# Kernel tuning notes

Measured on AMD Instinct MI355X. Metric: run time of the kernel, lower is better.

Reference implementation:

```python
import jax, jax.numpy as jnp
import numpy as np

B, S, D, P = 8, 2048, 512, 64  # batch, seq, num_embed_hidden, num_attention_project


def setup_inputs() -> dict:
    key = jax.random.key(0)
    ks = jax.random.split(key, 9)
    sd = 1.0 / np.sqrt(D)
    sp = 1.0 / np.sqrt(P)
    return {
        "query": jax.random.normal(ks[0], (B, S, D), dtype=jnp.float32),
        "attention_mask": jnp.ones((B, S), dtype=jnp.float32),
        "Wq": jax.random.uniform(ks[1], (D, P), jnp.float32, -sd, sd),
        "bq": jax.random.uniform(ks[2], (P,), jnp.float32, -sd, sd),
        "Wk": jax.random.uniform(ks[3], (D, P), jnp.float32, -sd, sd),
        "bk": jax.random.uniform(ks[4], (P,), jnp.float32, -sd, sd),
        "Wv": jax.random.uniform(ks[5], (D, P), jnp.float32, -sd, sd),
        "bv": jax.random.uniform(ks[6], (P,), jnp.float32, -sd, sd),
        "Wo": jax.random.uniform(ks[7], (P, D), jnp.float32, -sp, sp),
        "bo": jax.random.uniform(ks[8], (D,), jnp.float32, -sp, sp),
    }


def reference(query, attention_mask, Wq, bq, Wk, bk, Wv, bv, Wo, bo):
    q = jnp.einsum("bsd,dp->bsp", query, Wq) + bq  # [B,S,P]
    k = jnp.einsum("bsd,dp->bsp", query, Wk) + bk
    v = jnp.einsum("bsd,dp->bsp", query, Wv) + bv
    scores = jnp.einsum("bsp,btp->bst", q, k) / jnp.sqrt(jnp.float32(P))  # [B,S,S]
    # Faithful to original: mask broadcast over last axis via unsqueeze(-1) -> masks rows
    scores = scores + (1.0 - attention_mask[:, :, None]) * -10000.0
    weights = jax.nn.softmax(scores, axis=-1)
    weighted = jnp.einsum("bst,btp->bsp", weights, v)
    return jnp.einsum("bsp,pd->bsd", weighted, Wo) + bo
```

## Files before the change

kernel.cpp:

```cpp
#include <hip/hip_runtime.h>
#include <hip/hip_bf16.h>
#include <math.h>

constexpr int B = 8;
constexpr int S = 2048;
constexpr int D = 512;
constexpr int P = 64;
constexpr float SCALE = 0.125f;

typedef short bf16x8 __attribute__((ext_vector_type(8)));
typedef float f32x4 __attribute__((ext_vector_type(4)));
typedef unsigned int u32;

__device__ __forceinline__ unsigned short f2bf(float x) {
  __hip_bfloat16 h = __float2bfloat16(x);
  return __builtin_bit_cast(unsigned short, h);
}
__device__ __forceinline__ float bf2f(unsigned short u) {
  unsigned int v = (unsigned int)u << 16;
  return __builtin_bit_cast(float, v);
}


__global__ __launch_bounds__(256) void prep_w(
    const float* __restrict__ Wq, const float* __restrict__ Wk,
    const float* __restrict__ Wv, const float* __restrict__ Wo,
    unsigned short* __restrict__ Bfrag, unsigned short* __restrict__ Wofrag) {
  const int i = blockIdx.x * 256 + threadIdx.x;
  if (i < 192 * 512) {
    const int d = i / 192;
    const int n = i - d * 192;
    const float* W = (n < 64) ? Wq : (n < 128) ? Wk : Wv;
    const float val = W[d * 64 + (n & 63)];
    const int nt = n >> 4, l15 = n & 15;
    const int k16 = d >> 5, l4 = (d >> 3) & 3, j = d & 7;
    Bfrag[(((nt * 16 + k16) * 4 + l4) * 16 + l15) * 8 + j] = f2bf(val);
  }
  if (i < 64 * 512) {
    const int k = i >> 9;
    const int n = i & 511;
    const float val = Wo[k * 512 + n];
    const int ct = n >> 4, l15 = n & 15;
    const int h = k >> 5, l4 = (k >> 3) & 3, j = k & 7;
    Wofrag[(((ct * 2 + h) * 4 + l4) * 16 + l15) * 8 + j] = f2bf(val);
  }
}

__global__ __launch_bounds__(256, 4) void qkv_mfma(
    const float* __restrict__ query, const unsigned short* __restrict__ Bfrag,
    const float* __restrict__ bq, const float* __restrict__ bk,
    const float* __restrict__ bv, unsigned short* __restrict__ qfrag,
    unsigned short* __restrict__ kfrag, unsigned short* __restrict__ vfrag) {
  __shared__ __align__(16) unsigned short Aq[16 * 512];

  const int tid = threadIdx.x;
  const int w = tid >> 6;
  const int l = tid & 63;
  const int l15 = l & 15;
  const int l4 = l >> 4;
  const int s0 = blockIdx.x * 16;

  const float* qsrc = query + (size_t)s0 * D;
#pragma unroll
  for (int step = 0; step < 4; ++step) {
    const int row = step * 4 + w;
    const float* pf = qsrc + row * D + l * 8;
    const float4 x = *(const float4*)pf;
    const float4 y = *(const float4*)(pf + 4);
    bf16x8 u;
    u[0] = (short)f2bf(x.x); u[1] = (short)f2bf(x.y);
    u[2] = (short)f2bf(x.z); u[3] = (short)f2bf(x.w);
    u[4] = (short)f2bf(y.x); u[5] = (short)f2bf(y.y);
    u[6] = (short)f2bf(y.z); u[7] = (short)f2bf(y.w);
    *(bf16x8*)&Aq[row * 512 + ((l ^ (row & 7)) << 3)] = u;
  }
  __syncthreads();

  f32x4 acc[3];
#pragma unroll
  for (int nt = 0; nt < 3; ++nt) acc[nt] = (f32x4){0.f, 0.f, 0.f, 0.f};

#pragma unroll
  for (int k16 = 0; k16 < 16; ++k16) {
    const int aslot = (k16 * 4 + l4) ^ (l15 & 7);
    const bf16x8 af = *(const bf16x8*)&Aq[l15 * 512 + (aslot << 3)];
#pragma unroll
    for (int nt = 0; nt < 3; ++nt) {
      const int ntg = w * 3 + nt;
      const bf16x8 bf =
          *(const bf16x8*)(Bfrag + ((size_t)(ntg * 16 + k16) * 64 + l) * 8);
      acc[nt] = __builtin_amdgcn_mfma_f32_16x16x32_bf16(af, bf, acc[nt], 0, 0,
                                                        0);
    }
  }

  const int b = s0 >> 11;
  const size_t bbase = (size_t)b * (S * P);
#pragma unroll
  for (int nt = 0; nt < 3; ++nt) {
    const int col = w * 48 + nt * 16 + l15;
    const int mat = col >> 6;
    const int p = col & 63;
    const float bb = ((mat == 0) ? bq : (mat == 1) ? bk : bv)[p];
#pragma unroll
    for (int r = 0; r < 4; ++r) {
      const int s = s0 + l4 * 4 + r;
      const int t = s & 2047;
      const float vl = acc[nt][r] + bb;
      if (mat == 2) {
        const int tb = t >> 5, chv = (t >> 3) & 3, jv = t & 7;
        const int pcv = p >> 4, rowv = p & 15;
        vfrag[bbase + (((size_t)(tb * 4 + pcv) * 4 + chv) * 16 + rowv) * 8 +
              jv] = f2bf(vl);
      } else {
        const int tile = t >> 4, rowin = t & 15;
        const int h = p >> 5, chp = (p >> 3) & 3, j = p & 7;
        unsigned short* dst = (mat == 0) ? qfrag : kfrag;
        dst[bbase + (((size_t)(tile * 2 + h) * 4 + chp) * 16 + rowin) * 8 +
            j] = f2bf(mat == 0 ? vl * SCALE : vl);
      }
    }
  }
}

__global__ __launch_bounds__(512, 4) void attn_fused(
    const unsigned short* __restrict__ qfrag,
    const unsigned short* __restrict__ kfrag,
    const unsigned short* __restrict__ vfrag,
    const unsigned short* __restrict__ Wofrag, const float* __restrict__ bo,
    float* __restrict__ out) {
  __shared__ __align__(16) unsigned char smem[57344];
  __shared__ float l_s[8][32];

  const int tid = threadIdx.x;
  const int w = tid >> 6;
  const int lane = tid & 63;
  const int l15 = lane & 15;
  const int l4 = lane >> 4;
  const int qg = w & 1;
  const int th = w >> 1;

  const int blk = blockIdx.x;
  const int b = blk & 7;
  const int s0 = (blk >> 3) * 64;

  const size_t bbase = (size_t)b * (S * P);
  const unsigned short* qf = qfrag + bbase;
  const unsigned short* kf = kfrag + bbase;
  const unsigned short* vf = vfrag + bbase;

  unsigned short* e_s = (unsigned short*)smem + w * 2048;

  bf16x8 aq[2][2];
#pragma unroll
  for (int st = 0; st < 2; ++st)
#pragma unroll
    for (int h = 0; h < 2; ++h)
      aq[st][h] = *(const bf16x8*)(qf +
                                   ((size_t)(((s0 >> 4) + qg * 2 + st) * 2 + h) *
                                        64 +
                                    lane) *
                                       8);

  f32x4 acc[2][4];
#pragma unroll
  for (int st = 0; st < 2; ++st)
#pragma unroll
    for (int pc = 0; pc < 4; ++pc) acc[st][pc] = (f32x4){0.f, 0.f, 0.f, 0.f};
  float lpart[2][4] = {{0.f, 0.f, 0.f, 0.f}, {0.f, 0.f, 0.f, 0.f}};

  for (int win = 0; win < 8; ++win) {
    const int t0 = th * 512 + win * 64;

    bf16x8 bk[4][2];
#pragma unroll
    for (int nt = 0; nt < 4; ++nt)
#pragma unroll
      for (int h = 0; h < 2; ++h)
        bk[nt][h] =
            *(const bf16x8*)(kf +
                             ((size_t)(((t0 >> 4) + nt) * 2 + h) * 64 + lane) *
                                 8);

    f32x4 sc[2][4];
#pragma unroll
    for (int st = 0; st < 2; ++st)
#pragma unroll
      for (int nt = 0; nt < 4; ++nt) {
        f32x4 c = (f32x4){0.f, 0.f, 0.f, 0.f};
        c = __builtin_amdgcn_mfma_f32_16x16x32_bf16(aq[st][0], bk[nt][0], c, 0,
                                                    0, 0);
        sc[st][nt] = __builtin_amdgcn_mfma_f32_16x16x32_bf16(
            aq[st][1], bk[nt][1], c, 0, 0, 0);
      }

    bf16x8 bv[4][2];
#pragma unroll
    for (int pc = 0; pc < 4; ++pc)
#pragma unroll
      for (int kk = 0; kk < 2; ++kk)
        bv[pc][kk] =
            *(const bf16x8*)(vf +
                             ((size_t)(((t0 >> 5) + kk) * 4 + pc) * 64 + lane) *
                                 8);

#pragma unroll
    for (int st = 0; st < 2; ++st)
#pragma unroll
      for (int nt = 0; nt < 4; ++nt) {
        const int ch = nt * 2 + (l15 >> 3);
#pragma unroll
        for (int r = 0; r < 4; ++r) {
          const int rr = l4 * 4 + r;
          const unsigned short eu = f2bf(__expf(sc[st][nt][r]));
          lpart[st][r] += bf2f(eu);
          e_s[st * 1024 + rr * 64 + ((ch ^ (rr & 7)) << 3) + (l15 & 7)] = eu;
        }
      }

#pragma unroll
    for (int st = 0; st < 2; ++st) {
      bf16x8 ae[2];
#pragma unroll
      for (int kk = 0; kk < 2; ++kk)
        ae[kk] = *(const bf16x8*)&e_s[st * 1024 + l15 * 64 +
                                      (((kk * 4 + l4) ^ (l15 & 7)) << 3)];
#pragma unroll
      for (int pc = 0; pc < 4; ++pc) {
        acc[st][pc] = __builtin_amdgcn_mfma_f32_16x16x32_bf16(
            ae[0], bv[pc][0], acc[st][pc], 0, 0, 0);
        acc[st][pc] = __builtin_amdgcn_mfma_f32_16x16x32_bf16(
            ae[1], bv[pc][1], acc[st][pc], 0, 0, 0);
      }
    }
  }

#pragma unroll
  for (int st = 0; st < 2; ++st)
#pragma unroll
    for (int r = 0; r < 4; ++r) {
      float v = lpart[st][r];
      v += __shfl_xor(v, 1, 64);
      v += __shfl_xor(v, 2, 64);
      v += __shfl_xor(v, 4, 64);
      v += __shfl_xor(v, 8, 64);
      if (l15 == 0) l_s[w][st * 16 + l4 * 4 + r] = v;
    }

  __syncthreads();

  float* pacc = (float*)smem;
  if (th > 0) {
#pragma unroll
    for (int st = 0; st < 2; ++st)
#pragma unroll
      for (int pc = 0; pc < 4; ++pc)
#pragma unroll
        for (int r = 0; r < 4; ++r)
          pacc[((size_t)(qg * 3 + th - 1) * 32 + st * 16 + l4 * 4 + r) * 64 +
               pc * 16 + l15] = acc[st][pc][r];
  }
  __syncthreads();

  unsigned short* wnorm = (unsigned short*)(smem + 49152);
  if (th == 0) {
#pragma unroll
    for (int st = 0; st < 2; ++st) {
      float rl[4];
#pragma unroll
      for (int r = 0; r < 4; ++r) {
        const int row = st * 16 + l4 * 4 + r;
        rl[r] = 1.f / (l_s[qg][row] + l_s[2 + qg][row] + l_s[4 + qg][row] +
                       l_s[6 + qg][row]);
      }
#pragma unroll
      for (int pc = 0; pc < 4; ++pc)
#pragma unroll
        for (int r = 0; r < 4; ++r) {
          float s = acc[st][pc][r];
#pragma unroll
          for (int j = 0; j < 3; ++j)
            s += pacc[((size_t)(qg * 3 + j) * 32 + st * 16 + l4 * 4 + r) * 64 +
                      pc * 16 + l15];
          wnorm[(qg * 32 + st * 16 + l4 * 4 + r) * 64 + pc * 16 + l15] =
              f2bf(s * rl[r]);
        }
    }
  }
  __syncthreads();

  const int sub = w & 3;
  const int chalf = w >> 2;
  const bf16x8 a0 = *(const bf16x8*)&wnorm[(sub * 16 + l15) * 64 + l4 * 8];
  const bf16x8 a1 =
      *(const bf16x8*)&wnorm[(sub * 16 + l15) * 64 + 32 + l4 * 8];
  const size_t orow0 = (size_t)b * S + s0 + sub * 16;
#pragma unroll
  for (int ct = 0; ct < 16; ++ct) {
    const int ctg = chalf * 16 + ct;
    const bf16x8 b0 =
        *(const bf16x8*)(Wofrag + ((size_t)(ctg * 2 + 0) * 64 + lane) * 8);
    const bf16x8 b1 =
        *(const bf16x8*)(Wofrag + ((size_t)(ctg * 2 + 1) * 64 + lane) * 8);
    f32x4 c = (f32x4){0.f, 0.f, 0.f, 0.f};
    c = __builtin_amdgcn_mfma_f32_16x16x32_bf16(a0, b0, c, 0, 0, 0);
    c = __builtin_amdgcn_mfma_f32_16x16x32_bf16(a1, b1, c, 0, 0, 0);
    const int col = ctg * 16 + l15;
    const float bb = bo[col];
#pragma unroll
    for (int r = 0; r < 4; ++r)
      out[(orow0 + l4 * 4 + r) * D + col] = c[r] + bb;
  }
}

extern "C" void kernel_launch(void* const* d_in, const int* in_sizes, int n_in,
                              void* d_out, int out_size, void* d_ws,
                              size_t ws_size, hipStream_t stream) {
  const float* query = (const float*)d_in[0];
  const float* Wq = (const float*)d_in[2];
  const float* bq = (const float*)d_in[3];
  const float* Wk = (const float*)d_in[4];
  const float* bk = (const float*)d_in[5];
  const float* Wv = (const float*)d_in[6];
  const float* bv = (const float*)d_in[7];
  const float* Wo = (const float*)d_in[8];
  const float* bo = (const float*)d_in[9];
  float* out = (float*)d_out;

  const size_t proj = (size_t)B * S * P;
  unsigned short* qfr = (unsigned short*)d_ws;
  unsigned short* kfr = qfr + proj;
  unsigned short* vfr = kfr + proj;
  unsigned short* Bfrag = vfr + proj;
  unsigned short* Wofrag = Bfrag + 192 * 512;

  prep_w<<<384, 256, 0, stream>>>(Wq, Wk, Wv, Wo, Bfrag, Wofrag);
  qkv_mfma<<<1024, 256, 0, stream>>>(query, Bfrag, bq, bk, bv, qfr, kfr, vfr);
  attn_fused<<<256, 512, 0, stream>>>(qfr, kfr, vfr, Wofrag, bo, out);
}
```

Baseline: 142.4 us.

## Double attention block to 16 waves splitting keys eight ways, stagger access order

The attention kernel now runs 1024 threads per block, so 16 waves split each 64-query tile's keys eight ways instead of four. Each wave handles four 64-key windows and writes its exp tile into a double-buffered LDS region, with the score and exp steps interleaved per query subtile. Window order, QKV k-order and output column order are rotated per block to spread concurrent global/L2 accesses. LDS grows to about 128 KB per block, which limits residency to one block per CU and adds a larger cross-wave partial-sum reduction.

```diff
diff --git a/kernel.cpp b/kernel.cpp
--- a/kernel.cpp
+++ b/kernel.cpp
@@ -59,6 +59,7 @@
   const int l15 = l & 15;
   const int l4 = l >> 4;
   const int s0 = blockIdx.x * 16;
+  const int kb0 = blockIdx.x & 15;
 
   const float* qsrc = query + (size_t)s0 * D;
 #pragma unroll
@@ -81,7 +82,8 @@
   for (int nt = 0; nt < 3; ++nt) acc[nt] = (f32x4){0.f, 0.f, 0.f, 0.f};
 
 #pragma unroll
-  for (int k16 = 0; k16 < 16; ++k16) {
+  for (int kk = 0; kk < 16; ++kk) {
+    const int k16 = (kk + kb0) & 15;
     const int aslot = (k16 * 4 + l4) ^ (l15 & 7);
     const bf16x8 af = *(const bf16x8*)&Aq[l15 * 512 + (aslot << 3)];
 #pragma unroll
@@ -123,14 +125,14 @@
   }
 }
 
-__global__ __launch_bounds__(512, 4) void attn_fused(
+__global__ __launch_bounds__(1024, 4) void attn_fused(
     const unsigned short* __restrict__ qfrag,
     const unsigned short* __restrict__ kfrag,
     const unsigned short* __restrict__ vfrag,
     const unsigned short* __restrict__ Wofrag, const float* __restrict__ bo,
     float* __restrict__ out) {
-  __shared__ __align__(16) unsigned char smem[57344];
-  __shared__ float l_s[8][32];
+  __shared__ __align__(16) unsigned char smem[131072];
+  __shared__ float l_s[16][32];
 
   const int tid = threadIdx.x;
   const int w = tid >> 6;
@@ -142,25 +144,27 @@
 
   const int blk = blockIdx.x;
   const int b = blk & 7;
-  const int s0 = (blk >> 3) * 64;
+  const int qt = blk >> 3;
+  const int s0 = qt * 64;
+  const int wst = qt & 3;
 
   const size_t bbase = (size_t)b * (S * P);
   const unsigned short* qf = qfrag + bbase;
   const unsigned short* kf = kfrag + bbase;
   const unsigned short* vf = vfrag + bbase;
 
-  unsigned short* e_s = (unsigned short*)smem + w * 2048;
+  unsigned short* e_w = (unsigned short*)smem + w * 4096;
 
   bf16x8 aq[2][2];
 #pragma unroll
   for (int st = 0; st < 2; ++st)
 #pragma unroll
     for (int h = 0; h < 2; ++h)
-      aq[st][h] = *(const bf16x8*)(qf +
-                                   ((size_t)(((s0 >> 4) + qg * 2 + st) * 2 + h) *
-                                        64 +
-                                    lane) *
-                                       8);
+      aq[st][h] =
+          *(const bf16x8*)(qf +
+                           ((size_t)(((s0 >> 4) + qg * 2 + st) * 2 + h) * 64 +
+                            lane) *
+                               8);
 
   f32x4 acc[2][4];
 #pragma unroll
@@ -169,8 +173,10 @@
     for (int pc = 0; pc < 4; ++pc) acc[st][pc] = (f32x4){0.f, 0.f, 0.f, 0.f};
   float lpart[2][4] = {{0.f, 0.f, 0.f, 0.f}, {0.f, 0.f, 0.f, 0.f}};
 
-  for (int win = 0; win < 8; ++win) {
-    const int t0 = th * 512 + win * 64;
+  for (int win = 0; win < 4; ++win) {
+    const int wi = (win + wst) & 3;
+    const int t0 = th * 256 + wi * 64;
+    unsigned short* e_s = e_w + (win & 1) * 2048;
 
     bf16x8 bk[4][2];
 #pragma unroll
@@ -182,17 +188,29 @@
                              ((size_t)(((t0 >> 4) + nt) * 2 + h) * 64 + lane) *
                                  8);
 
-    f32x4 sc[2][4];
-#pragma unroll
-    for (int st = 0; st < 2; ++st)
+#pragma unroll
+    for (int st = 0; st < 2; ++st) {
+      f32x4 sc[4];
 #pragma unroll
       for (int nt = 0; nt < 4; ++nt) {
         f32x4 c = (f32x4){0.f, 0.f, 0.f, 0.f};
         c = __builtin_amdgcn_mfma_f32_16x16x32_bf16(aq[st][0], bk[nt][0], c, 0,
                                                     0, 0);
-        sc[st][nt] = __builtin_amdgcn_mfma_f32_16x16x32_bf16(
-            aq[st][1], bk[nt][1], c, 0, 0, 0);
-      }
+        sc[nt] = __builtin_amdgcn_mfma_f32_16x16x32_bf16(aq[st][1], bk[nt][1],
+                                                         c, 0, 0, 0);
+      }
+#pragma unroll
+      for (int nt = 0; nt < 4; ++nt) {
+        const int ch = nt * 2 + (l15 >> 3);
+#pragma unroll
+        for (int r = 0; r < 4; ++r) {
+          const int rr = l4 * 4 + r;
+          const unsigned short eu = f2bf(__expf(sc[nt][r]));
+          lpart[st][r] += bf2f(eu);
+          e_s[st * 1024 + rr * 64 + ((ch ^ (rr & 7)) << 3) + (l15 & 7)] = eu;
+        }
+      }
+    }
 
     bf16x8 bv[4][2];
 #pragma unroll
@@ -203,20 +221,6 @@
             *(const bf16x8*)(vf +
                              ((size_t)(((t0 >> 5) + kk) * 4 + pc) * 64 + lane) *
                                  8);
-
-#pragma unroll
-    for (int st = 0; st < 2; ++st)
-#pragma unroll
-      for (int nt = 0; nt < 4; ++nt) {
-        const int ch = nt * 2 + (l15 >> 3);
-#pragma unroll
-        for (int r = 0; r < 4; ++r) {
-          const int rr = l4 * 4 + r;
-          const unsigned short eu = f2bf(__expf(sc[st][nt][r]));
-          lpart[st][r] += bf2f(eu);
-          e_s[st * 1024 + rr * 64 + ((ch ^ (rr & 7)) << 3) + (l15 & 7)] = eu;
-        }
-      }
 
 #pragma unroll
     for (int st = 0; st < 2; ++st) {
@@ -257,12 +261,12 @@
       for (int pc = 0; pc < 4; ++pc)
 #pragma unroll
         for (int r = 0; r < 4; ++r)
-          pacc[((size_t)(qg * 3 + th - 1) * 32 + st * 16 + l4 * 4 + r) * 64 +
+          pacc[((size_t)(qg * 7 + th - 1) * 32 + st * 16 + l4 * 4 + r) * 64 +
                pc * 16 + l15] = acc[st][pc][r];
   }
   __syncthreads();
 
-  unsigned short* wnorm = (unsigned short*)(smem + 49152);
+  unsigned short* wnorm = (unsigned short*)(smem + 114688);
   if (th == 0) {
 #pragma unroll
     for (int st = 0; st < 2; ++st) {
@@ -270,8 +274,10 @@
 #pragma unroll
       for (int r = 0; r < 4; ++r) {
         const int row = st * 16 + l4 * 4 + r;
-        rl[r] = 1.f / (l_s[qg][row] + l_s[2 + qg][row] + l_s[4 + qg][row] +
-                       l_s[6 + qg][row]);
+        float ls = 0.f;
+#pragma unroll
+        for (int t8 = 0; t8 < 8; ++t8) ls += l_s[t8 * 2 + qg][row];
+        rl[r] = 1.f / ls;
       }
 #pragma unroll
       for (int pc = 0; pc < 4; ++pc)
@@ -279,8 +285,8 @@
         for (int r = 0; r < 4; ++r) {
           float s = acc[st][pc][r];
 #pragma unroll
-          for (int j = 0; j < 3; ++j)
-            s += pacc[((size_t)(qg * 3 + j) * 32 + st * 16 + l4 * 4 + r) * 64 +
+          for (int j = 0; j < 7; ++j)
+            s += pacc[((size_t)(qg * 7 + j) * 32 + st * 16 + l4 * 4 + r) * 64 +
                       pc * 16 + l15];
           wnorm[(qg * 32 + st * 16 + l4 * 4 + r) * 64 + pc * 16 + l15] =
               f2bf(s * rl[r]);
@@ -290,14 +296,14 @@
   __syncthreads();
 
   const int sub = w & 3;
-  const int chalf = w >> 2;
+  const int chq = w >> 2;
   const bf16x8 a0 = *(const bf16x8*)&wnorm[(sub * 16 + l15) * 64 + l4 * 8];
   const bf16x8 a1 =
       *(const bf16x8*)&wnorm[(sub * 16 + l15) * 64 + 32 + l4 * 8];
   const size_t orow0 = (size_t)b * S + s0 + sub * 16;
 #pragma unroll
-  for (int ct = 0; ct < 16; ++ct) {
-    const int ctg = chalf * 16 + ct;
+  for (int ct = 0; ct < 8; ++ct) {
+    const int ctg = chq * 8 + ((ct + (blk & 7)) & 7);
     const bf16x8 b0 =
         *(const bf16x8*)(Wofrag + ((size_t)(ctg * 2 + 0) * 64 + lane) * 8);
     const bf16x8 b1 =
@@ -336,5 +342,5 @@
 
   prep_w<<<384, 256, 0, stream>>>(Wq, Wk, Wv, Wo, Bfrag, Wofrag);
   qkv_mfma<<<1024, 256, 0, stream>>>(query, Bfrag, bq, bk, bv, qfr, kfr, vfr);
-  attn_fused<<<256, 512, 0, stream>>>(qfr, kfr, vfr, Wofrag, bo, out);
-}
+  attn_fused<<<256, 1024, 0, stream>>>(qfr, kfr, vfr, Wofrag, bo, out);
+}
```

Result: no change. 139.9 us (-1.8%).
